# Performance work log

Measured on AMD Instinct MI355X. Metric: run time of the kernel, lower is better.

The kernel has to match this reference:

```python
import jax, jax.numpy as jnp
import numpy as np

N, E, G = 50000, 800000, 512
EMB, HID, NSHAPE, NCOLOR, NCLS = 128, 256, 64, 64, 32


def setup_inputs() -> dict:
    key = jax.random.key(0)
    ks = jax.random.split(key, 12)
    s = 0.05
    return {
        "x": jax.random.randint(ks[0], (N, 2), 0, NSHAPE),
        "edge_index": jax.random.randint(ks[1], (2, E), 0, N),
        "batch": jnp.sort(jax.random.randint(ks[2], (N,), 0, G)),
        "shape_emb": jax.random.normal(ks[3], (NSHAPE, EMB)) * s,
        "color_emb": jax.random.normal(ks[4], (NCOLOR, EMB)) * s,
        # SAGEConv: lin_l (applied to aggregated neighbors, with bias), lin_r (root, no bias)
        "w1l": jax.random.normal(ks[5], (HID, 2 * EMB)) * s,
        "b1l": jnp.zeros((HID,)),
        "w1r": jax.random.normal(ks[6], (HID, 2 * EMB)) * s,
        "w2l": jax.random.normal(ks[7], (HID, HID)) * s,
        "b2l": jnp.zeros((HID,)),
        "w2r": jax.random.normal(ks[8], (HID, HID)) * s,
        "wc": jax.random.normal(ks[9], (NCLS, HID)) * s,
        "bc": jnp.zeros((NCLS,)),
    }


def _sage_conv(h, src, dst, wl, bl, wr):
    # mean-aggregate messages h[src] onto dst, then lin_l(aggr) + lin_r(h)
    msg = h[src]  # [E, d]
    agg = jax.ops.segment_sum(msg, dst, num_segments=N)  # [N, d]
    deg = jax.ops.segment_sum(jnp.ones((src.shape[0],), h.dtype), dst, num_segments=N)
    agg = agg / jnp.maximum(deg, 1.0)[:, None]
    return agg @ wl.T + bl + h @ wr.T


def reference(x, edge_index, batch, shape_emb, color_emb,
              w1l, b1l, w1r, w2l, b2l, w2r, wc, bc):
    src, dst = edge_index[0], edge_index[1]
    h = jnp.concatenate([shape_emb[x[:, 0]], color_emb[x[:, 1]]], axis=-1)  # [N, 2*EMB]
    h = jax.nn.relu(_sage_conv(h, src, dst, w1l, b1l, w1r))
    h = jax.nn.relu(_sage_conv(h, src, dst, w2l, b2l, w2r))
    # global mean pool over graphs
    hs = jax.ops.segment_sum(h, batch, num_segments=G)  # [G, HID]
    cnt = jax.ops.segment_sum(jnp.ones((N,), h.dtype), batch, num_segments=G)
    hg = hs / jnp.maximum(cnt, 1.0)[:, None]
    return hg @ wc.T + bc  # [G, NCLS]
```

## Files before the change

### kernel.cpp

```cpp
#include <hip/hip_runtime.h>
#include <hip/hip_bf16.h>


#define EMB   128
#define HID   256
#define NCLS  32
#define DIM   256

typedef __attribute__((ext_vector_type(8))) short short8v;
typedef __attribute__((ext_vector_type(4))) float float4v;

__device__ __forceinline__ unsigned short f2bf(float f) {
    unsigned int u = __float_as_uint(f);
    unsigned int r = u + 0x7FFFu + ((u >> 16) & 1u);
    return (unsigned short)(r >> 16);
}
__device__ __forceinline__ float bf2f(unsigned short s) {
    return __uint_as_float(((unsigned int)s) << 16);
}

__global__ void build_bq2(const float* __restrict__ w1l, const float* __restrict__ w1r,
                          const float* __restrict__ w2l, const float* __restrict__ w2r,
                          unsigned short* __restrict__ b1hi, unsigned short* __restrict__ b1lo,
                          unsigned short* __restrict__ b2hi, unsigned short* __restrict__ b2lo) {
    int tid = blockIdx.x * 256 + threadIdx.x;
    int which = tid >> 17;
    int r = tid & 0x1FFFF;
    int k = r >> 8, o = r & 255;
    const float* wl = which ? w2l : w1l;
    const float* wr = which ? w2r : w1r;
    float v = (k < 256) ? wl[o * 256 + k] : wr[o * 256 + (k - 256)];
    unsigned short h = f2bf(v);
    unsigned short l = f2bf(v - bf2f(h));
    int idx = (((k >> 3) * 256) + o) * 8 + (k & 7);
    (which ? b2hi : b1hi)[idx] = h;
    (which ? b2lo : b1lo)[idx] = l;
}

__global__ void embed_bf16(const int* __restrict__ x,
                           const float* __restrict__ se, const float* __restrict__ ce,
                           unsigned short* __restrict__ hb, unsigned short* __restrict__ hf,
                           int n_nodes) {
    int tid = blockIdx.x * 256 + threadIdx.x;
    if (tid >= n_nodes * 32) return;
    int n = tid >> 5, c = tid & 31;
    const float* src = (c < 16) ? (se + (size_t)x[n * 2] * EMB + c * 8)
                                : (ce + (size_t)x[n * 2 + 1] * EMB + (c - 16) * 8);
    float4 v0 = *(const float4*)src;
    float4 v1 = *(const float4*)(src + 4);
    ushort4 o0 = make_ushort4(f2bf(v0.x), f2bf(v0.y), f2bf(v0.z), f2bf(v0.w));
    ushort4 o1 = make_ushort4(f2bf(v1.x), f2bf(v1.y), f2bf(v1.z), f2bf(v1.w));
    *(ushort4*)(hb + (size_t)tid * 8)     = o0;
    *(ushort4*)(hb + (size_t)tid * 8 + 4) = o1;
    size_t fo = ((size_t)(n >> 4) * 32 + c) * 128 + (n & 15) * 8;
    *(ushort4*)(hf + fo)     = o0;
    *(ushort4*)(hf + fo + 4) = o1;
}


__global__ void count_deg(const int* __restrict__ dst, int* __restrict__ deg, int E) {
    int e = blockIdx.x * 256 + threadIdx.x;
    if (e < E) atomicAdd(&deg[dst[e]], 1);
}

__global__ void scan_block(const int* __restrict__ deg, int* __restrict__ rowptr,
                           int* __restrict__ bsums, int n) {
    __shared__ int s[256];
    int t = threadIdx.x;
    int i = blockIdx.x * 256 + t;
    int v = (i < n) ? deg[i] : 0;
    s[t] = v; __syncthreads();
    for (int off = 1; off < 256; off <<= 1) {
        int x = (t >= off) ? s[t - off] : 0;
        __syncthreads(); s[t] += x; __syncthreads();
    }
    if (i < n) rowptr[i] = s[t] - v;
    if (t == 255) bsums[blockIdx.x] = s[255];
}

__global__ void scan_sums(int* __restrict__ bsums, int nb, int* __restrict__ rowptr,
                          int n, int E) {
    __shared__ int s[256];
    int t = threadIdx.x;
    int v = (t < nb) ? bsums[t] : 0;
    s[t] = v; __syncthreads();
    for (int off = 1; off < 256; off <<= 1) {
        int x = (t >= off) ? s[t - off] : 0;
        __syncthreads(); s[t] += x; __syncthreads();
    }
    if (t < nb) bsums[t] = s[t] - v;
    if (t == 0) rowptr[n] = E;
}

__global__ void scan_add(int* __restrict__ rowptr, const int* __restrict__ bsums, int n) {
    int i = blockIdx.x * 256 + threadIdx.x;
    if (i < n) rowptr[i] += bsums[i >> 8];
}

__global__ void fill_csr(const int* __restrict__ src, const int* __restrict__ dst,
                         const int* __restrict__ rowptr, int* __restrict__ cursor,
                         int* __restrict__ csr, int E) {
    int e = blockIdx.x * 256 + threadIdx.x;
    if (e >= E) return;
    int d = dst[e];
    int pos = rowptr[d] + atomicAdd(&cursor[d], 1);
    csr[pos] = src[e];
}

__global__ void aggregate_bf16(const unsigned short* __restrict__ hb,
                               const int* __restrict__ rowptr, const int* __restrict__ csr,
                               unsigned short* __restrict__ ahiF, unsigned short* __restrict__ aloF,
                               int n_nodes) {
    int wid = (blockIdx.x * 256 + threadIdx.x) >> 6;
    int lane = threadIdx.x & 63;
    if (wid >= n_nodes) return;
    int beg = rowptr[wid], end = rowptr[wid + 1];
    float a0 = 0.f, a1 = 0.f, a2 = 0.f, a3 = 0.f;
    int k = beg;
    for (; k + 3 < end; k += 4) {
        int s0 = csr[k], s1 = csr[k + 1], s2 = csr[k + 2], s3 = csr[k + 3];
        ushort4 u0 = *(const ushort4*)(hb + (size_t)s0 * DIM + lane * 4);
        ushort4 u1 = *(const ushort4*)(hb + (size_t)s1 * DIM + lane * 4);
        ushort4 u2 = *(const ushort4*)(hb + (size_t)s2 * DIM + lane * 4);
        ushort4 u3 = *(const ushort4*)(hb + (size_t)s3 * DIM + lane * 4);
        a0 += bf2f(u0.x) + bf2f(u1.x) + bf2f(u2.x) + bf2f(u3.x);
        a1 += bf2f(u0.y) + bf2f(u1.y) + bf2f(u2.y) + bf2f(u3.y);
        a2 += bf2f(u0.z) + bf2f(u1.z) + bf2f(u2.z) + bf2f(u3.z);
        a3 += bf2f(u0.w) + bf2f(u1.w) + bf2f(u2.w) + bf2f(u3.w);
    }
    for (; k < end; ++k) {
        ushort4 u = *(const ushort4*)(hb + (size_t)csr[k] * DIM + lane * 4);
        a0 += bf2f(u.x); a1 += bf2f(u.y); a2 += bf2f(u.z); a3 += bf2f(u.w);
    }
    int d = end - beg;
    float inv = 1.0f / (float)(d > 1 ? d : 1);
    float v[4] = {a0 * inv, a1 * inv, a2 * inv, a3 * inv};
    unsigned short hs[4], ls[4];
#pragma unroll
    for (int i = 0; i < 4; ++i) {
        hs[i] = f2bf(v[i]);
        ls[i] = f2bf(v[i] - bf2f(hs[i]));
    }
    size_t base = ((size_t)(wid >> 4) * 32 + (lane >> 1)) * 128 + (wid & 15) * 8 + (lane & 1) * 4;
    *(ushort4*)(ahiF + base) = make_ushort4(hs[0], hs[1], hs[2], hs[3]);
    *(ushort4*)(aloF + base) = make_ushort4(ls[0], ls[1], ls[2], ls[3]);
}

__global__ void __launch_bounds__(256, 3)
gemm_mfma(const unsigned short* __restrict__ Ahi, const unsigned short* __restrict__ Alo,
          const unsigned short* __restrict__ Hf,
          const unsigned short* __restrict__ Bhi, const unsigned short* __restrict__ Blo,
          const float* __restrict__ bias,
          float* __restrict__ Houtf, unsigned short* __restrict__ Houtb,
          unsigned short* __restrict__ Hfrag, int M) {
    const int t = threadIdx.x;
    const int w = t >> 6, lane = t & 63;
    const int lrow = lane & 15, koct = lane >> 4;
    const int wm = w >> 1, wn = w & 1;
    const int rb = blockIdx.y * 128 + wm * 64;
    const int cb = blockIdx.x * 64 + wn * 32;
    const int mbmax = (M >> 4) - 1;

    size_t abase[4];
#pragma unroll
    for (int mt = 0; mt < 4; ++mt) {
        int mb = (rb >> 4) + mt;
        if (mb > mbmax) mb = mbmax;
        abase[mt] = (size_t)mb * 32 * 128 + lrow * 8;
    }
    const int col0 = cb + lrow;

    float4v acc[4][2];
#pragma unroll
    for (int i = 0; i < 4; ++i)
#pragma unroll
        for (int j = 0; j < 2; ++j) acc[i][j] = (float4v){0.f, 0.f, 0.f, 0.f};

#pragma unroll 2
    for (int kt = 0; kt < 8; ++kt) {
        const size_t kof = (size_t)(kt * 4 + koct) * 128;
        const int kg = kt * 4 + koct;
        short8v ah[4], al[4], bh[2], bl[2];
#pragma unroll
        for (int mt = 0; mt < 4; ++mt) {
            ah[mt] = *(const short8v*)(Ahi + abase[mt] + kof);
            al[mt] = *(const short8v*)(Alo + abase[mt] + kof);
        }
#pragma unroll
        for (int nt = 0; nt < 2; ++nt) {
            size_t bofs = ((size_t)kg * 256 + col0 + nt * 16) * 8;
            bh[nt] = *(const short8v*)(Bhi + bofs);
            bl[nt] = *(const short8v*)(Blo + bofs);
        }
#pragma unroll
        for (int mt = 0; mt < 4; ++mt)
#pragma unroll
            for (int nt = 0; nt < 2; ++nt) {
                acc[mt][nt] = __builtin_amdgcn_mfma_f32_16x16x32_bf16(ah[mt], bh[nt], acc[mt][nt], 0, 0, 0);
                acc[mt][nt] = __builtin_amdgcn_mfma_f32_16x16x32_bf16(ah[mt], bl[nt], acc[mt][nt], 0, 0, 0);
                acc[mt][nt] = __builtin_amdgcn_mfma_f32_16x16x32_bf16(al[mt], bh[nt], acc[mt][nt], 0, 0, 0);
            }
    }

#pragma unroll 2
    for (int kt = 0; kt < 8; ++kt) {
        const size_t kof = (size_t)(kt * 4 + koct) * 128;
        const int kg = (kt + 8) * 4 + koct;
        short8v ah[4], bh[2], bl[2];
#pragma unroll
        for (int mt = 0; mt < 4; ++mt)
            ah[mt] = *(const short8v*)(Hf + abase[mt] + kof);
#pragma unroll
        for (int nt = 0; nt < 2; ++nt) {
            size_t bofs = ((size_t)kg * 256 + col0 + nt * 16) * 8;
            bh[nt] = *(const short8v*)(Bhi + bofs);
            bl[nt] = *(const short8v*)(Blo + bofs);
        }
#pragma unroll
        for (int mt = 0; mt < 4; ++mt)
#pragma unroll
            for (int nt = 0; nt < 2; ++nt) {
                acc[mt][nt] = __builtin_amdgcn_mfma_f32_16x16x32_bf16(ah[mt], bh[nt], acc[mt][nt], 0, 0, 0);
                acc[mt][nt] = __builtin_amdgcn_mfma_f32_16x16x32_bf16(ah[mt], bl[nt], acc[mt][nt], 0, 0, 0);
            }
    }

    float bv[2];
#pragma unroll
    for (int nt = 0; nt < 2; ++nt) bv[nt] = bias[cb + nt * 16 + lrow];

#pragma unroll
    for (int mt = 0; mt < 4; ++mt) {
#pragma unroll
        for (int r = 0; r < 4; ++r) {
            int grow = rb + mt * 16 + koct * 4 + r;
            if (grow >= M) continue;
            size_t fbase = ((size_t)(grow >> 4) * 32) * 128 + (grow & 15) * 8;
#pragma unroll
            for (int nt = 0; nt < 2; ++nt) {
                float vv = fmaxf(acc[mt][nt][r] + bv[nt], 0.f);
                int col = cb + nt * 16 + lrow;
                if (Houtf) Houtf[(size_t)grow * DIM + col] = vv;
                if (Houtb) Houtb[(size_t)grow * DIM + col] = f2bf(vv);
                if (Hfrag) Hfrag[fbase + (size_t)(col >> 3) * 128 + (col & 7)] = f2bf(vv);
            }
        }
    }
}


__global__ void pool_kernel(const float* __restrict__ h, const int* __restrict__ batch,
                            float* __restrict__ hg, int n_nodes) {
    int g = blockIdx.x;
    int t = threadIdx.x;
    int lo = 0, hi = n_nodes;
    while (lo < hi) { int mid = (lo + hi) >> 1; if (batch[mid] < g) lo = mid + 1; else hi = mid; }
    int start = lo;
    hi = n_nodes;
    while (lo < hi) { int mid = (lo + hi) >> 1; if (batch[mid] < g + 1) lo = mid + 1; else hi = mid; }
    int end = lo;
    float acc = 0.f;
    for (int n = start; n < end; ++n) acc += h[(size_t)n * DIM + t];
    int c = end - start;
    hg[g * DIM + t] = acc / (float)(c > 1 ? c : 1);
}

__global__ void head_kernel(const float* __restrict__ hg, const float* __restrict__ wc,
                            const float* __restrict__ bc, float* __restrict__ out, int total) {
    int tid = blockIdx.x * 256 + threadIdx.x;
    if (tid >= total) return;
    int g = tid >> 5, c = tid & 31;
    const float* hr = hg + (size_t)g * DIM;
    const float* wr = wc + (size_t)c * DIM;
    float acc = bc[c];
    for (int k = 0; k < DIM; ++k) acc = fmaf(hr[k], wr[k], acc);
    out[tid] = acc;
}


extern "C" void kernel_launch(void* const* d_in, const int* in_sizes, int n_in,
                              void* d_out, int out_size, void* d_ws, size_t ws_size,
                              hipStream_t stream) {
    const int* x      = (const int*)d_in[0];
    const int* ei     = (const int*)d_in[1];
    const int* batch  = (const int*)d_in[2];
    const float* se   = (const float*)d_in[3];
    const float* ce   = (const float*)d_in[4];
    const float* w1l  = (const float*)d_in[5];
    const float* b1l  = (const float*)d_in[6];
    const float* w1r  = (const float*)d_in[7];
    const float* w2l  = (const float*)d_in[8];
    const float* b2l  = (const float*)d_in[9];
    const float* w2r  = (const float*)d_in[10];
    const float* wc   = (const float*)d_in[11];
    const float* bc   = (const float*)d_in[12];
    float* out = (float*)d_out;

    const int N = in_sizes[0] / 2;
    const int E = in_sizes[1] / 2;
    const int G = out_size / NCLS;
    const int* src = ei;
    const int* dst = ei + E;

    float* h2 = (float*)d_ws;
    unsigned short* agghiF = (unsigned short*)(h2 + (size_t)N * DIM);
    unsigned short* aggloF = agghiF + (size_t)N * DIM;
    unsigned short* h0b    = aggloF + (size_t)N * DIM;
    unsigned short* h0f    = h0b + (size_t)N * DIM;
    unsigned short* h1b    = h0f + (size_t)N * DIM;
    unsigned short* h1f    = h1b + (size_t)N * DIM;
    unsigned short* B1hi   = h1f + (size_t)N * DIM;
    unsigned short* B1lo   = B1hi + 131072;
    unsigned short* B2hi   = B1lo + 131072;
    unsigned short* B2lo   = B2hi + 131072;
    float* hg  = (float*)(B2lo + 131072);
    int* deg    = (int*)(hg + (size_t)G * DIM);
    int* rowptr = deg + N;
    int* cursor = rowptr + (N + 1);
    int* csr    = cursor + N;
    int* bsums  = csr + E;

    hipMemsetAsync(deg, 0, (size_t)(3 * N + 1) * sizeof(int), stream);

    embed_bf16<<<(N * 32 + 255) / 256, 256, 0, stream>>>(x, se, ce, h0b, h0f, N);

    int eblocks = (E + 255) / 256;
    count_deg<<<eblocks, 256, 0, stream>>>(dst, deg, E);
    int sblocks = (N + 255) / 256;
    scan_block<<<sblocks, 256, 0, stream>>>(deg, rowptr, bsums, N);
    scan_sums<<<1, 256, 0, stream>>>(bsums, sblocks, rowptr, N, E);
    scan_add<<<sblocks, 256, 0, stream>>>(rowptr, bsums, N);
    fill_csr<<<eblocks, 256, 0, stream>>>(src, dst, rowptr, cursor, csr, E);

    build_bq2<<<1024, 256, 0, stream>>>(w1l, w1r, w2l, w2r, B1hi, B1lo, B2hi, B2lo);

    dim3 ggrid(256 / 64, (N + 127) / 128);
    int ablocks = (N * 64 + 255) / 256;

    aggregate_bf16<<<ablocks, 256, 0, stream>>>(h0b, rowptr, csr, agghiF, aggloF, N);
    gemm_mfma<<<ggrid, 256, 0, stream>>>(agghiF, aggloF, h0f, B1hi, B1lo, b1l,
                                         nullptr, h1b, h1f, N);

    aggregate_bf16<<<ablocks, 256, 0, stream>>>(h1b, rowptr, csr, agghiF, aggloF, N);
    gemm_mfma<<<ggrid, 256, 0, stream>>>(agghiF, aggloF, h1f, B2hi, B2lo, b2l,
                                         h2, nullptr, nullptr, N);

    pool_kernel<<<G, 256, 0, stream>>>(h2, batch, hg, N);
    head_kernel<<<(G * NCLS + 255) / 256, 256, 0, stream>>>(hg, wc, bc, out, G * NCLS);
}
```

Measured before the change: 536.4 us.

## Stage A tiles in LDS and give each GEMM block full output width

```diff
diff --git a/kernel.cpp b/kernel.cpp
--- a/kernel.cpp
+++ b/kernel.cpp
@@ -146,45 +146,58 @@
     *(ushort4*)(aloF + base) = make_ushort4(ls[0], ls[1], ls[2], ls[3]);
 }
 
-__global__ void __launch_bounds__(256, 3)
+__global__ void __launch_bounds__(512, 4)
 gemm_mfma(const unsigned short* __restrict__ Ahi, const unsigned short* __restrict__ Alo,
           const unsigned short* __restrict__ Hf,
           const unsigned short* __restrict__ Bhi, const unsigned short* __restrict__ Blo,
           const float* __restrict__ bias,
           float* __restrict__ Houtf, unsigned short* __restrict__ Houtb,
           unsigned short* __restrict__ Hfrag, int M) {
+    __shared__ __align__(16) unsigned short lds_a[32768];
+
     const int t = threadIdx.x;
     const int w = t >> 6, lane = t & 63;
     const int lrow = lane & 15, koct = lane >> 4;
-    const int wm = w >> 1, wn = w & 1;
-    const int rb = blockIdx.y * 128 + wm * 64;
-    const int cb = blockIdx.x * 64 + wn * 32;
+    const int m0 = blockIdx.x * 64;
+    const int nw = w * 32;
     const int mbmax = (M >> 4) - 1;
 
+#pragma unroll
+    for (int i = 0; i < 8; ++i) {
+        int rb = i & 3;
+        int mb = (m0 >> 4) + rb;
+        if (mb > mbmax) mb = mbmax;
+        const unsigned short* srcp = ((i < 4) ? Ahi : Alo) + (size_t)mb * 4096 + t * 8;
+        *(short8v*)&lds_a[((i < 4) ? 0 : 16384) + rb * 4096 + t * 8] =
+            *(const short8v*)srcp;
+    }
+
     size_t abase[4];
 #pragma unroll
     for (int mt = 0; mt < 4; ++mt) {
-        int mb = (rb >> 4) + mt;
+        int mb = (m0 >> 4) + mt;
         if (mb > mbmax) mb = mbmax;
         abase[mt] = (size_t)mb * 32 * 128 + lrow * 8;
     }
-    const int col0 = cb + lrow;
+    const int col0 = nw + lrow;
 
     float4v acc[4][2];
 #pragma unroll
     for (int i = 0; i < 4; ++i)
 #pragma unroll
         for (int j = 0; j < 2; ++j) acc[i][j] = (float4v){0.f, 0.f, 0.f, 0.f};
+
+    __syncthreads();
 
 #pragma unroll 2
     for (int kt = 0; kt < 8; ++kt) {
-        const size_t kof = (size_t)(kt * 4 + koct) * 128;
+        const int kof = (kt * 4 + koct) * 128 + lrow * 8;
         const int kg = kt * 4 + koct;
         short8v ah[4], al[4], bh[2], bl[2];
 #pragma unroll
         for (int mt = 0; mt < 4; ++mt) {
-            ah[mt] = *(const short8v*)(Ahi + abase[mt] + kof);
-            al[mt] = *(const short8v*)(Alo + abase[mt] + kof);
+            ah[mt] = *(const short8v*)&lds_a[mt * 4096 + kof];
+            al[mt] = *(const short8v*)&lds_a[16384 + mt * 4096 + kof];
         }
 #pragma unroll
         for (int nt = 0; nt < 2; ++nt) {
@@ -227,19 +240,19 @@
 
     float bv[2];
 #pragma unroll
-    for (int nt = 0; nt < 2; ++nt) bv[nt] = bias[cb + nt * 16 + lrow];
+    for (int nt = 0; nt < 2; ++nt) bv[nt] = bias[nw + nt * 16 + lrow];
 
 #pragma unroll
     for (int mt = 0; mt < 4; ++mt) {
 #pragma unroll
         for (int r = 0; r < 4; ++r) {
-            int grow = rb + mt * 16 + koct * 4 + r;
+            int grow = m0 + mt * 16 + koct * 4 + r;
             if (grow >= M) continue;
             size_t fbase = ((size_t)(grow >> 4) * 32) * 128 + (grow & 15) * 8;
 #pragma unroll
             for (int nt = 0; nt < 2; ++nt) {
                 float vv = fmaxf(acc[mt][nt][r] + bv[nt], 0.f);
-                int col = cb + nt * 16 + lrow;
+                int col = nw + nt * 16 + lrow;
                 if (Houtf) Houtf[(size_t)grow * DIM + col] = vv;
                 if (Houtb) Houtb[(size_t)grow * DIM + col] = f2bf(vv);
                 if (Hfrag) Hfrag[fbase + (size_t)(col >> 3) * 128 + (col & 7)] = f2bf(vv);
@@ -334,16 +347,16 @@
 
     build_bq2<<<1024, 256, 0, stream>>>(w1l, w1r, w2l, w2r, B1hi, B1lo, B2hi, B2lo);
 
-    dim3 ggrid(256 / 64, (N + 127) / 128);
+    int gblocks = (N + 63) / 64;
     int ablocks = (N * 64 + 255) / 256;
 
     aggregate_bf16<<<ablocks, 256, 0, stream>>>(h0b, rowptr, csr, agghiF, aggloF, N);
-    gemm_mfma<<<ggrid, 256, 0, stream>>>(agghiF, aggloF, h0f, B1hi, B1lo, b1l,
-                                         nullptr, h1b, h1f, N);
+    gemm_mfma<<<gblocks, 512, 0, stream>>>(agghiF, aggloF, h0f, B1hi, B1lo, b1l,
+                                           nullptr, h1b, h1f, N);
 
     aggregate_bf16<<<ablocks, 256, 0, stream>>>(h1b, rowptr, csr, agghiF, aggloF, N);
-    gemm_mfma<<<ggrid, 256, 0, stream>>>(agghiF, aggloF, h1f, B2hi, B2lo, b2l,
-                                         h2, nullptr, nullptr, N);
+    gemm_mfma<<<gblocks, 512, 0, stream>>>(agghiF, aggloF, h1f, B2hi, B2lo, b2l,
+                                           h2, nullptr, nullptr, N);
 
     pool_kernel<<<G, 256, 0, stream>>>(h2, batch, hg, N);
     head_kernel<<<(G * NCLS + 255) / 256, 256, 0, stream>>>(hg, wc, bc, out, G * NCLS);
```

After: 472.6 us. 1.13x faster.
